# Kernel tuning notes

Measured on AMD Instinct MI355X. Metric: run time of the kernel, lower is better.

## Reference

```python
import jax, jax.numpy as jnp
import numpy as np

N_HEAD = 16
EPS = 1e-6


def _rope(x, cos, sin):
    # x: [B, T, H, D]; cos/sin: [1, T, 1, D//2]
    d = x.shape[-1] // 2
    x1, x2 = x[..., :d], x[..., d:]
    return jnp.concatenate([x1 * cos + x2 * sin, -x1 * sin + x2 * cos], axis=-1)


def _rmsnorm(x):
    # parameter-free RMSNorm over last dim
    return x * jax.lax.rsqrt(jnp.mean(x * x, axis=-1, keepdims=True) + EPS)


def setup_inputs() -> dict:
    key = jax.random.key(0)
    ks = jax.random.split(key, 5)
    B, T, C = 4, 2048, 1024
    d_half = (C // N_HEAD) // 2
    x = jax.random.normal(ks[0], (B, T, C), dtype=jnp.float32)
    # realistic rotary tables
    inv_freq = 1.0 / (10000.0 ** (np.arange(d_half, dtype=np.float32) / d_half))
    t = np.arange(T, dtype=np.float32)
    freqs = np.outer(t, inv_freq)  # [T, d_half]
    cos = jnp.asarray(np.cos(freqs))[None, :, None, :]
    sin = jnp.asarray(np.sin(freqs))[None, :, None, :]
    w_attn = jax.random.normal(ks[1], (3 * C, C), dtype=jnp.float32) * 0.02
    w_proj = jax.random.normal(ks[2], (C, C), dtype=jnp.float32) * 0.02
    return {"x": x, "cos": cos, "sin": sin, "w_attn": w_attn, "w_proj": w_proj}


def reference(x, cos, sin, w_attn, w_proj):
    B, T, C = x.shape
    H = N_HEAD
    D = C // H
    qkv = x @ w_attn.T  # [B, T, 3C]
    q, k, v = jnp.split(qkv, 3, axis=2)
    q = q.reshape(B, T, H, D)
    k = k.reshape(B, T, H, D)
    v = v.reshape(B, T, H, D)
    q = _rmsnorm(_rope(q, cos, sin))
    k = _rmsnorm(_rope(k, cos, sin))
    # causal SDPA
    scale = 1.0 / jnp.sqrt(jnp.asarray(D, dtype=x.dtype))
    scores = jnp.einsum("bqhd,bkhd->bhqk", q, k) * scale  # [B, H, T, T]
    causal = jnp.tril(jnp.ones((T, T), dtype=bool))
    scores = jnp.where(causal[None, None], scores, jnp.asarray(-jnp.inf, dtype=scores.dtype))
    att = jax.nn.softmax(scores, axis=-1)
    y = jnp.einsum("bhqk,bkhd->bqhd", att, v).reshape(B, T, C)
    return y @ w_proj.T
```

## Files before the change

### kernel.cpp

```cpp
#include <hip/hip_runtime.h>
#include <hip/hip_bf16.h>
#include <math.h>


#define TT 2048
#define CC 1024
#define HH 16
#define DD 64

typedef __attribute__((ext_vector_type(8))) short short8;
typedef __attribute__((ext_vector_type(4))) short short4_t;
typedef __attribute__((ext_vector_type(4))) float f32x4;
typedef unsigned short ushort_t;

__device__ __forceinline__ ushort_t f2bf(float f) {
    unsigned u = __builtin_bit_cast(unsigned, f);
    u = (u + 0x7fffu + ((u >> 16) & 1u)) >> 16;
    return (ushort_t)u;
}

__global__ __launch_bounds__(256) void cast_bf16(const float* __restrict__ in,
                                                 ushort_t* __restrict__ out, int n8) {
    const int i = blockIdx.x * 256 + threadIdx.x;
    if (i >= n8) return;
    const float4* p = (const float4*)in + (size_t)i * 2;
    float4 f0 = p[0], f1 = p[1];
    short8 v;
    v[0] = (short)f2bf(f0.x); v[1] = (short)f2bf(f0.y);
    v[2] = (short)f2bf(f0.z); v[3] = (short)f2bf(f0.w);
    v[4] = (short)f2bf(f1.x); v[5] = (short)f2bf(f1.y);
    v[6] = (short)f2bf(f1.z); v[7] = (short)f2bf(f1.w);
    *(short8*)(out + (size_t)i * 8) = v;
}

template <bool OUTF32>
__global__ __launch_bounds__(256) void gemm_bt(const ushort_t* __restrict__ A,
                                               const ushort_t* __restrict__ B,
                                               void* __restrict__ C,
                                               int M, int N, int K, int lda) {
    __shared__ ushort_t As[2][128 * 32];
    __shared__ ushort_t Bs[2][128 * 32];

    const int tid  = threadIdx.x;
    const int wv   = tid >> 6;
    const int ln   = tid & 63;
    const int quad = ln >> 4;
    const int lm   = ln & 15;
    const int wm   = wv & 1;
    const int wn   = wv >> 1;
    const int rowC = blockIdx.y * 128;
    const int colC = blockIdx.x * 128;

    const int srow = wv * 16 + (ln >> 2);
    const int skq  = (ln & 3) * 8;

    f32x4 acc[4][4];
#pragma unroll
    for (int i = 0; i < 4; ++i)
#pragma unroll
        for (int j = 0; j < 4; ++j) acc[i][j] = (f32x4){0.f, 0.f, 0.f, 0.f};

    auto stage = [&](int k0, int bufi) {
#pragma unroll
        for (int half = 0; half < 2; ++half) {
            const ushort_t* gA = A + (size_t)(rowC + half * 64 + srow) * lda + k0 + skq;
            const ushort_t* gB = B + (size_t)(colC + half * 64 + srow) * K + k0 + skq;
            ushort_t* lA = As[bufi] + (half * 64 + wv * 16) * 32;
            ushort_t* lB = Bs[bufi] + (half * 64 + wv * 16) * 32;
            __builtin_amdgcn_global_load_lds(
                (const __attribute__((address_space(1))) unsigned int*)gA,
                (__attribute__((address_space(3))) unsigned int*)lA, 16, 0, 0);
            __builtin_amdgcn_global_load_lds(
                (const __attribute__((address_space(1))) unsigned int*)gB,
                (__attribute__((address_space(3))) unsigned int*)lB, 16, 0, 0);
        }
    };

    stage(0, 0);
    __syncthreads();

    int cur = 0;
    for (int k0 = 0; k0 < K; k0 += 32) {
        if (k0 + 32 < K) stage(k0 + 32, cur ^ 1);

        short8 af[4], bf[4];
#pragma unroll
        for (int mt = 0; mt < 4; ++mt)
            af[mt] = *(const short8*)&As[cur][(wm * 64 + mt * 16 + lm) * 32 + quad * 8];
#pragma unroll
        for (int nt = 0; nt < 4; ++nt)
            bf[nt] = *(const short8*)&Bs[cur][(wn * 64 + nt * 16 + lm) * 32 + quad * 8];
#pragma unroll
        for (int mt = 0; mt < 4; ++mt)
#pragma unroll
            for (int nt = 0; nt < 4; ++nt)
                acc[mt][nt] = __builtin_amdgcn_mfma_f32_16x16x32_bf16(
                    af[mt], bf[nt], acc[mt][nt], 0, 0, 0);

        __syncthreads();
        cur ^= 1;
    }

#pragma unroll
    for (int mt = 0; mt < 4; ++mt)
#pragma unroll
        for (int r = 0; r < 4; ++r) {
            const size_t row = rowC + wm * 64 + mt * 16 + quad * 4 + r;
#pragma unroll
            for (int nt = 0; nt < 4; ++nt) {
                const size_t col = colC + wn * 64 + nt * 16 + lm;
                if (OUTF32) ((float*)C)[row * N + col] = acc[mt][nt][r];
                else        ((ushort_t*)C)[row * N + col] = f2bf(acc[mt][nt][r]);
            }
        }
}

__global__ __launch_bounds__(256) void gemm_qkv(const ushort_t* __restrict__ A,
                                                const ushort_t* __restrict__ B,
                                                ushort_t* __restrict__ C,
                                                ushort_t* __restrict__ vtb,
                                                const float* __restrict__ cosb,
                                                const float* __restrict__ sinb,
                                                int M, int N, int K) {
    __shared__ ushort_t As[2][128 * 32];
    __shared__ ushort_t Bs[2][128 * 32];

    const int tid  = threadIdx.x;
    const int wv   = tid >> 6;
    const int ln   = tid & 63;
    const int quad = ln >> 4;
    const int lm   = ln & 15;
    const int wm   = wv & 1;
    const int wn   = wv >> 1;
    const int rowC = blockIdx.y * 128;
    const int colC = blockIdx.x * 128;

    const int srow = wv * 16 + (ln >> 2);
    const int skq  = (ln & 3) * 8;

    f32x4 acc[4][4];
#pragma unroll
    for (int i = 0; i < 4; ++i)
#pragma unroll
        for (int j = 0; j < 4; ++j) acc[i][j] = (f32x4){0.f, 0.f, 0.f, 0.f};

    auto stage = [&](int k0, int bufi) {
#pragma unroll
        for (int half = 0; half < 2; ++half) {
            const ushort_t* gA = A + (size_t)(rowC + half * 64 + srow) * K + k0 + skq;
            const ushort_t* gB = B + (size_t)(colC + half * 64 + srow) * K + k0 + skq;
            ushort_t* lA = As[bufi] + (half * 64 + wv * 16) * 32;
            ushort_t* lB = Bs[bufi] + (half * 64 + wv * 16) * 32;
            __builtin_amdgcn_global_load_lds(
                (const __attribute__((address_space(1))) unsigned int*)gA,
                (__attribute__((address_space(3))) unsigned int*)lA, 16, 0, 0);
            __builtin_amdgcn_global_load_lds(
                (const __attribute__((address_space(1))) unsigned int*)gB,
                (__attribute__((address_space(3))) unsigned int*)lB, 16, 0, 0);
        }
    };

    stage(0, 0);
    __syncthreads();

    int cur = 0;
    for (int k0 = 0; k0 < K; k0 += 32) {
        if (k0 + 32 < K) stage(k0 + 32, cur ^ 1);

        short8 af[4], bf[4];
#pragma unroll
        for (int mt = 0; mt < 4; ++mt)
            af[mt] = *(const short8*)&As[cur][(wm * 64 + mt * 16 + lm) * 32 + quad * 8];
#pragma unroll
        for (int nt = 0; nt < 4; ++nt)
            bf[nt] = *(const short8*)&Bs[cur][(wn * 64 + nt * 16 + lm) * 32 + quad * 8];
#pragma unroll
        for (int mt = 0; mt < 4; ++mt)
#pragma unroll
            for (int nt = 0; nt < 4; ++nt)
                acc[mt][nt] = __builtin_amdgcn_mfma_f32_16x16x32_bf16(
                    af[mt], bf[nt], acc[mt][nt], 0, 0, 0);

        __syncthreads();
        cur ^= 1;
    }

    const bool isqk = colC < 2 * CC;
    if (isqk) {
#pragma unroll
        for (int mt = 0; mt < 4; ++mt)
#pragma unroll
            for (int r = 0; r < 4; ++r) {
                const int row = rowC + wm * 64 + mt * 16 + quad * 4 + r;
                ushort_t* Cp = C + (size_t)row * N + colC + wn * 64 + lm;
                const int t = row & (TT - 1);
                float ss = 0.f;
#pragma unroll
                for (int nt = 0; nt < 4; ++nt) ss += acc[mt][nt][r] * acc[mt][nt][r];
                ss += __shfl_xor(ss, 1);
                ss += __shfl_xor(ss, 2);
                ss += __shfl_xor(ss, 4);
                ss += __shfl_xor(ss, 8);
                const float rinv = rsqrtf(ss * (1.0f / 64.0f) + 1e-6f);
                const float c0 = cosb[t * 32 + lm];
                const float c1 = cosb[t * 32 + 16 + lm];
                const float s0 = sinb[t * 32 + lm];
                const float s1 = sinb[t * 32 + 16 + lm];
                const float o0 = acc[mt][0][r] * c0 + acc[mt][2][r] * s0;
                const float o1 = acc[mt][1][r] * c1 + acc[mt][3][r] * s1;
                const float o2 = acc[mt][2][r] * c0 - acc[mt][0][r] * s0;
                const float o3 = acc[mt][3][r] * c1 - acc[mt][1][r] * s1;
                Cp[0]  = f2bf(o0 * rinv);
                Cp[16] = f2bf(o1 * rinv);
                Cp[32] = f2bf(o2 * rinv);
                Cp[48] = f2bf(o3 * rinv);
            }
    } else {
#pragma unroll
        for (int mt = 0; mt < 4; ++mt) {
            const int row0 = rowC + wm * 64 + mt * 16 + quad * 4;
            const int bb = row0 >> 11;
            const int tt = row0 & (TT - 1);
#pragma unroll
            for (int nt = 0; nt < 4; ++nt) {
                const int hd = colC - 2 * CC + wn * 64 + nt * 16 + lm;
                short4_t pk;
                pk[0] = (short)f2bf(acc[mt][nt][0]);
                pk[1] = (short)f2bf(acc[mt][nt][1]);
                pk[2] = (short)f2bf(acc[mt][nt][2]);
                pk[3] = (short)f2bf(acc[mt][nt][3]);
                *(short4_t*)(vtb + (size_t)(bb * CC + hd) * TT + tt) = pk;
            }
        }
    }
}

__global__ __launch_bounds__(256, 3) void attn_mfma(ushort_t* __restrict__ qkv,
                                                    const ushort_t* __restrict__ vt) {
    const int bx = blockIdx.x;
    const int c  = 15 - (bx >> 6);
    const int hb = bx & 63;
    const int h  = hb & 15;
    const int b  = hb >> 4;
    const int tid  = threadIdx.x;
    const int w    = tid >> 6;
    const int lane = tid & 63;
    const int quad = lane >> 4;
    const int lm   = lane & 15;

    __shared__ ushort_t Ks[2][64][72];
    __shared__ ushort_t Vs[2][64][72];

    short8 qf[2][2];
#pragma unroll
    for (int qs = 0; qs < 2; ++qs) {
        const ushort_t* qa = qkv + (size_t)(b * TT + c * 128 + w * 32 + qs * 16 + lm) * (3 * CC) + h * DD;
        qf[qs][0] = *(const short8*)(qa + quad * 8);
        qf[qs][1] = *(const short8*)(qa + 32 + quad * 8);
    }

    f32x4 O[2][4];
    f32x4 lac[2];
#pragma unroll
    for (int qs = 0; qs < 2; ++qs) {
        lac[qs] = (f32x4){0.f, 0.f, 0.f, 0.f};
#pragma unroll
        for (int dt = 0; dt < 4; ++dt) O[qs][dt] = (f32x4){0.f, 0.f, 0.f, 0.f};
    }

    const short one_bf = (short)0x3F80;
    const short8 vones = {one_bf, one_bf, one_bf, one_bf, one_bf, one_bf, one_bf, one_bf};

    const int sn = tid >> 2;
    const int si = tid & 3;
    const int sd = si * 16;
    const int kb = ((si >> 1) << 5) + ((si & 1) << 2);

    short8 k0v, k1v, v0v, v1v;
    auto stage_load = [&](int kt) {
        const ushort_t* kp = qkv + (size_t)(b * TT + kt * 64 + sn) * (3 * CC) + CC + h * DD + sd;
        k0v = *(const short8*)kp;
        k1v = *(const short8*)(kp + 8);
        const ushort_t* vp = vt + (size_t)(b * CC + h * DD + sn) * TT + kt * 64 + sd;
        v0v = *(const short8*)vp;
        v1v = *(const short8*)(vp + 8);
    };
    auto stage_write = [&](int bufi) {
        *(short8*)&Ks[bufi][sn][sd]     = k0v;
        *(short8*)&Ks[bufi][sn][sd + 8] = k1v;
        *(short4_t*)&Vs[bufi][sn][kb]      = __builtin_shufflevector(v0v, v0v, 0, 1, 2, 3);
        *(short4_t*)&Vs[bufi][sn][kb + 8]  = __builtin_shufflevector(v0v, v0v, 4, 5, 6, 7);
        *(short4_t*)&Vs[bufi][sn][kb + 16] = __builtin_shufflevector(v1v, v1v, 0, 1, 2, 3);
        *(short4_t*)&Vs[bufi][sn][kb + 24] = __builtin_shufflevector(v1v, v1v, 4, 5, 6, 7);
    };

    const int ktmax = 2 * c + 1;
    const int ktw   = 2 * c + (w >> 1);
    const int qoff  = (w & 1) * 32;

    stage_load(0);
    stage_write(0);
    __syncthreads();

    int cur = 0;
    for (int kt = 0; kt <= ktmax; ++kt) {
        if (kt < ktmax) stage_load(kt + 1);

        if (kt <= ktw) {
            short8 kf[2][4], vf[2][4];
#pragma unroll
            for (int kk = 0; kk < 2; ++kk)
#pragma unroll
                for (int i = 0; i < 4; ++i) {
                    kf[kk][i] = *(const short8*)&Ks[cur][i * 16 + lm][kk * 32 + quad * 8];
                    vf[kk][i] = *(const short8*)&Vs[cur][i * 16 + lm][kk * 32 + quad * 8];
                }
            const bool diag = (kt == ktw);

#pragma unroll
            for (int qs = 0; qs < 2; ++qs) {
                f32x4 sf[4];
#pragma unroll
                for (int i = 0; i < 4; ++i) sf[i] = (f32x4){0.f, 0.f, 0.f, 0.f};
#pragma unroll
                for (int kk = 0; kk < 2; ++kk)
#pragma unroll
                    for (int i = 0; i < 4; ++i)
                        sf[i] = __builtin_amdgcn_mfma_f32_16x16x32_bf16(
                            kf[kk][i], qf[qs][kk], sf[i], 0, 0, 0);

                short8 pa0 = {0, 0, 0, 0, 0, 0, 0, 0};
                short8 pa1 = {0, 0, 0, 0, 0, 0, 0, 0};
#pragma unroll
                for (int i = 0; i < 4; ++i)
#pragma unroll
                    for (int r = 0; r < 4; ++r) {
                        const float s = fmaf(sf[i][r], 0.125f, -8.0f);
                        float p = __expf(s);
                        if (diag) {
                            const int kloc = i * 16 + quad * 4 + r;
                            p = (kloc <= qoff + qs * 16 + lm) ? p : 0.0f;
                        }
                        const short pb = (short)f2bf(p);
                        if (i < 2) pa0[(i & 1) * 4 + r] = pb;
                        else       pa1[(i & 1) * 4 + r] = pb;
                    }

#pragma unroll
                for (int dt = 0; dt < 4; ++dt)
                    O[qs][dt] = __builtin_amdgcn_mfma_f32_16x16x32_bf16(
                        pa0, vf[0][dt], O[qs][dt], 0, 0, 0);
                lac[qs] = __builtin_amdgcn_mfma_f32_16x16x32_bf16(
                    pa0, vones, lac[qs], 0, 0, 0);
#pragma unroll
                for (int dt = 0; dt < 4; ++dt)
                    O[qs][dt] = __builtin_amdgcn_mfma_f32_16x16x32_bf16(
                        pa1, vf[1][dt], O[qs][dt], 0, 0, 0);
                lac[qs] = __builtin_amdgcn_mfma_f32_16x16x32_bf16(
                    pa1, vones, lac[qs], 0, 0, 0);
            }
        }

        if (kt < ktmax) stage_write(cur ^ 1);
        __syncthreads();
        cur ^= 1;
    }

#pragma unroll
    for (int qs = 0; qs < 2; ++qs)
#pragma unroll
        for (int r = 0; r < 4; ++r) {
            const float inv_l = 1.0f / lac[qs][r];
            ushort_t* yp = qkv + (size_t)(b * TT + c * 128 + w * 32 + qs * 16 + quad * 4 + r) * (3 * CC)
                               + 2 * CC + h * DD + lm;
#pragma unroll
            for (int dt = 0; dt < 4; ++dt) yp[dt * 16] = f2bf(O[qs][dt][r] * inv_l);
        }
}

extern "C" void kernel_launch(void* const* d_in, const int* in_sizes, int n_in,
                              void* d_out, int out_size, void* d_ws, size_t ws_size,
                              hipStream_t stream) {
    const float* x      = (const float*)d_in[0];
    const float* cosb   = (const float*)d_in[1];
    const float* sinb   = (const float*)d_in[2];
    const float* w_attn = (const float*)d_in[3];
    const float* w_proj = (const float*)d_in[4];
    float* out = (float*)d_out;

    ushort_t* qkvb = (ushort_t*)d_ws;
    ushort_t* vtb  = qkvb + (size_t)8192 * 3072;
    ushort_t* xb   = vtb  + (size_t)8192 * 1024;
    ushort_t* wab  = xb   + (size_t)8192 * 1024;
    ushort_t* wpb  = wab  + (size_t)3072 * 1024;

    cast_bf16<<<(8192 * 1024 / 8 + 255) / 256, 256, 0, stream>>>(x, xb, 8192 * 1024 / 8);
    cast_bf16<<<(3072 * 1024 / 8 + 255) / 256, 256, 0, stream>>>(w_attn, wab, 3072 * 1024 / 8);
    cast_bf16<<<(1024 * 1024 / 8 + 255) / 256, 256, 0, stream>>>(w_proj, wpb, 1024 * 1024 / 8);

    gemm_qkv<<<dim3(3072 / 128, 8192 / 128), 256, 0, stream>>>(
        xb, wab, qkvb, vtb, cosb, sinb, 8192, 3072, 1024);

    attn_mfma<<<dim3(1024, 1, 1), 256, 0, stream>>>(qkvb, vtb);

    gemm_bt<true><<<dim3(1024 / 128, 8192 / 128), 256, 0, stream>>>(
        qkvb + 2 * CC, wpb, out, 8192, 1024, 1024, 3 * CC);
}
```

Baseline: 253.9 us.

## Triple-buffer GEMM LDS staging with partial vmcnt waits for deeper prefetch

Result: no change. 251.7 us (-0.9%).

```diff
diff --git a/kernel.cpp b/kernel.cpp
--- a/kernel.cpp
+++ b/kernel.cpp
@@ -38,8 +38,8 @@
                                                const ushort_t* __restrict__ B,
                                                void* __restrict__ C,
                                                int M, int N, int K, int lda) {
-    __shared__ ushort_t As[2][128 * 32];
-    __shared__ ushort_t Bs[2][128 * 32];
+    __shared__ ushort_t As[3][128 * 32];
+    __shared__ ushort_t Bs[3][128 * 32];
 
     const int tid  = threadIdx.x;
     const int wv   = tid >> 6;
@@ -76,12 +76,20 @@
         }
     };
 
+    const int nk = K >> 5;
     stage(0, 0);
-    __syncthreads();
+    stage(32, 1);
+    asm volatile("s_waitcnt vmcnt(4)" ::: "memory");
+    __builtin_amdgcn_sched_barrier(0);
+    __builtin_amdgcn_s_barrier();
 
     int cur = 0;
-    for (int k0 = 0; k0 < K; k0 += 32) {
-        if (k0 + 32 < K) stage(k0 + 32, cur ^ 1);
+    for (int ki = 0; ki < nk; ++ki) {
+        const bool has2 = (ki + 2 < nk);
+        if (has2) {
+            int b2 = cur + 2; if (b2 >= 3) b2 -= 3;
+            stage((ki + 2) << 5, b2);
+        }
 
         short8 af[4], bf[4];
 #pragma unroll
@@ -97,8 +105,11 @@
                 acc[mt][nt] = __builtin_amdgcn_mfma_f32_16x16x32_bf16(
                     af[mt], bf[nt], acc[mt][nt], 0, 0, 0);
 
-        __syncthreads();
-        cur ^= 1;
+        if (has2) { asm volatile("s_waitcnt vmcnt(4)" ::: "memory"); }
+        else      { asm volatile("s_waitcnt vmcnt(0)" ::: "memory"); }
+        __builtin_amdgcn_sched_barrier(0);
+        __builtin_amdgcn_s_barrier();
+        cur = (cur == 2) ? 0 : cur + 1;
     }
 
 #pragma unroll
@@ -122,8 +133,8 @@
                                                 const float* __restrict__ cosb,
                                                 const float* __restrict__ sinb,
                                                 int M, int N, int K) {
-    __shared__ ushort_t As[2][128 * 32];
-    __shared__ ushort_t Bs[2][128 * 32];
+    __shared__ ushort_t As[3][128 * 32];
+    __shared__ ushort_t Bs[3][128 * 32];
 
     const int tid  = threadIdx.x;
     const int wv   = tid >> 6;
@@ -160,12 +171,20 @@
         }
     };
 
+    const int nk = K >> 5;
     stage(0, 0);
-    __syncthreads();
+    stage(32, 1);
+    asm volatile("s_waitcnt vmcnt(4)" ::: "memory");
+    __builtin_amdgcn_sched_barrier(0);
+    __builtin_amdgcn_s_barrier();
 
     int cur = 0;
-    for (int k0 = 0; k0 < K; k0 += 32) {
-        if (k0 + 32 < K) stage(k0 + 32, cur ^ 1);
+    for (int ki = 0; ki < nk; ++ki) {
+        const bool has2 = (ki + 2 < nk);
+        if (has2) {
+            int b2 = cur + 2; if (b2 >= 3) b2 -= 3;
+            stage((ki + 2) << 5, b2);
+        }
 
         short8 af[4], bf[4];
 #pragma unroll
@@ -181,8 +200,11 @@
                 acc[mt][nt] = __builtin_amdgcn_mfma_f32_16x16x32_bf16(
                     af[mt], bf[nt], acc[mt][nt], 0, 0, 0);
 
-        __syncthreads();
-        cur ^= 1;
+        if (has2) { asm volatile("s_waitcnt vmcnt(4)" ::: "memory"); }
+        else      { asm volatile("s_waitcnt vmcnt(0)" ::: "memory"); }
+        __builtin_amdgcn_sched_barrier(0);
+        __builtin_amdgcn_s_barrier();
+        cur = (cur == 2) ? 0 : cur + 1;
     }
 
     const bool isqk = colC < 2 * CC;
```
